# Performance work log

Hardware: AMD Instinct MI355X
Metric: run time of the kernel (lower is better)

The kernel has to match this reference:

```python
import jax, jax.numpy as jnp
import numpy as np

EPS = 1e-5

def layer_norm(x, gamma, beta):
    mu = jnp.mean(x, axis=-1, keepdims=True)
    var = jnp.var(x, axis=-1, keepdims=True)
    return (x - mu) * jax.lax.rsqrt(var + EPS) * gamma + beta

def setup_inputs() -> dict:
    key = jax.random.key(0)
    ks = jax.random.split(key, 9)
    B, S, H = 4, 4096, 1024
    x = jax.random.normal(ks[0], (B, S, H), dtype=jnp.float32)
    w1 = jax.random.normal(ks[1], (H, 4 * H), dtype=jnp.float32) * (1.0 / np.sqrt(H))
    b1 = jnp.zeros((4 * H,), dtype=jnp.float32)
    w2 = jax.random.normal(ks[2], (4 * H, H), dtype=jnp.float32) * (1.0 / np.sqrt(4 * H))
    b2 = jnp.zeros((H,), dtype=jnp.float32)
    g1 = jnp.ones((H,), dtype=jnp.float32)
    be1 = jnp.zeros((H,), dtype=jnp.float32)
    g2 = jnp.ones((H,), dtype=jnp.float32)
    be2 = jnp.zeros((H,), dtype=jnp.float32)
    return {"x": x, "w1": w1, "b1": b1, "w2": w2, "b2": b2,
            "g1": g1, "be1": be1, "g2": g2, "be2": be2}

def reference(x, w1, b1, w2, b2, g1, be1, g2, be2):
    # FNet mixing: FFT over hidden dim, then seq dim, take real part
    x_ft = jnp.fft.fft(jnp.fft.fft(x.astype(jnp.float32), axis=-1), axis=-2).real
    h = layer_norm(x + x_ft, g1, be1)
    # FFN with exact GELU (torch nn.GELU default); dropout is identity in eval
    ffn = jax.nn.gelu(h @ w1 + b1, approximate=False) @ w2 + b2
    return layer_norm(h + ffn, g2, be2)
```

## Files before the change

kernel.cpp:

```cpp
#include <hip/hip_runtime.h>
#include <math.h>
#include <stdint.h>

#define DI __device__ __forceinline__
typedef unsigned short u16;
typedef unsigned int   u32;
typedef unsigned long long u64;

typedef __attribute__((ext_vector_type(4))) float f32x4;
typedef __attribute__((ext_vector_type(8))) short bf16x8;

DI float bf2f(u16 v){ return __uint_as_float(((u32)v) << 16); }
DI u16 f2bf(float f){ u32 u = __float_as_uint(f); return (u16)((u + 0x7FFFu + ((u >> 16) & 1u)) >> 16); }
DI u32 pack2(float re, float im){ return (u32)f2bf(re) | ((u32)f2bf(im) << 16); }

DI float gelu_fast(float v){
  float t = v * v;
  float z = v * fmaf(0.0356774081f, t, 0.7978845608f);
  z = fminf(z, 15.0f);
  float e = __expf(2.0f * z);
  return v * e * __frcp_rn(1.0f + e);
}

__global__ __launch_bounds__(256) void transpose_u32(const u32* __restrict__ in, u32* __restrict__ out, int R, int C){
  __shared__ u32 tile[64][65];
  int t = threadIdx.x;
  int c = t & 63, r0 = t >> 6;
  size_t bofs = (size_t)blockIdx.z * (size_t)R * (size_t)C;
  const u32* ib = in  + bofs + (size_t)(blockIdx.y * 64) * C + blockIdx.x * 64;
  u32*       ob = out + bofs + (size_t)(blockIdx.x * 64) * R + blockIdx.y * 64;
  #pragma unroll
  for (int i = 0; i < 16; i++){ int r = r0 + i * 4; tile[r][c] = ib[(size_t)r * C + c]; }
  __syncthreads();
  #pragma unroll
  for (int i = 0; i < 16; i++){ int r = r0 + i * 4; ob[(size_t)r * R + c] = tile[c][r]; }
}

__global__ __launch_bounds__(256) void transpose_f32_bf16(const float* __restrict__ in, u16* __restrict__ out, int R, int C){
  __shared__ u16 tile[64][65];
  int t = threadIdx.x;
  int c = t & 63, r0 = t >> 6;
  const float* ib = in  + (size_t)(blockIdx.y * 64) * C + blockIdx.x * 64;
  u16*         ob = out + (size_t)(blockIdx.x * 64) * R + blockIdx.y * 64;
  #pragma unroll
  for (int i = 0; i < 16; i++){ int r = r0 + i * 4; tile[r][c] = f2bf(ib[(size_t)r * C + c]); }
  __syncthreads();
  #pragma unroll
  for (int i = 0; i < 16; i++){ int r = r0 + i * 4; ob[(size_t)r * R + c] = tile[c][r]; }
}

template<int LOGN>
DI float2* fft_r4(float2* s, float2* d, int t){
  const int Q = 1 << (LOGN - 2);
  #pragma unroll
  for (int st = 0; st < (LOGN >> 1); ++st){
    const int m = 1 << (2 * st);
    const float ang = -6.28318530717958647692f * (float)m / (float)(1 << LOGN);
    #pragma unroll
    for (int j0 = 0; j0 < Q; j0 += 256){
      int j = j0 + t;
      int p = j >> (2 * st);
      int q = j & (m - 1);
      int o = q + (p << (2 * st + 2));
      float2 a0 = s[j], a1 = s[j + Q], a2 = s[j + 2 * Q], a3 = s[j + 3 * Q];
      float s0r = a0.x + a2.x, s0i = a0.y + a2.y, d0r = a0.x - a2.x, d0i = a0.y - a2.y;
      float s1r = a1.x + a3.x, s1i = a1.y + a3.y, d1r = a1.x - a3.x, d1i = a1.y - a3.y;
      float sn, cs; __sincosf(ang * (float)p, &sn, &cs);
      float t2r = cs * cs - sn * sn, t2i = 2.f * cs * sn;
      float t3r = t2r * cs - t2i * sn, t3i = t2r * sn + t2i * cs;
      float e1r = d0r + d1i, e1i = d0i - d1r;
      float e2r = s0r - s1r, e2i = s0i - s1i;
      float e3r = d0r - d1i, e3i = d0i + d1r;
      d[o]         = make_float2(s0r + s1r, s0i + s1i);
      d[o + m]     = make_float2(cs * e1r - sn * e1i,  cs * e1i + sn * e1r);
      d[o + 2 * m] = make_float2(t2r * e2r - t2i * e2i, t2r * e2i + t2i * e2r);
      d[o + 3 * m] = make_float2(t3r * e3r - t3i * e3i, t3r * e3i + t3i * e3r);
    }
    __syncthreads();
    float2* tp = s; s = d; d = tp;
  }
  return s;
}

__global__ __launch_bounds__(256) void fft_seq(const float* __restrict__ xT, u32* __restrict__ ZT2,
                                               float* __restrict__ Zny){
  __shared__ float2 A[4096], Bb[4096];
  int t = threadIdx.x, g = blockIdx.x;
  const float* r0 = xT + (size_t)(2 * g) * 4096;
  #pragma unroll
  for (int i = 0; i < 4; i++){
    int idx = i * 1024 + t * 4;
    float4 va = *(const float4*)(r0 + idx);
    float4 vb = *(const float4*)(r0 + 4096 + idx);
    A[idx + 0] = make_float2(va.x, vb.x);
    A[idx + 1] = make_float2(va.y, vb.y);
    A[idx + 2] = make_float2(va.z, vb.z);
    A[idx + 3] = make_float2(va.w, vb.w);
  }
  __syncthreads();
  float2* R = fft_r4<12>(A, Bb, t);
  size_t ob0 = (size_t)(2 * g) * 2048;
  #pragma unroll
  for (int i = 0; i < 2; i++){
    int k0 = i * 1024 + t * 4;
    u32 wa[4], wb[4];
    #pragma unroll
    for (int kk = 0; kk < 4; kk++){
      int k = k0 + kk, m = (4096 - k) & 4095;
      float2 zk = R[k], zm = R[m];
      wa[kk] = pack2(0.5f * (zk.x + zm.x), 0.5f * (zk.y - zm.y));
      wb[kk] = pack2(0.5f * (zk.y + zm.y), 0.5f * (zm.x - zk.x));
    }
    *(uint4*)(ZT2 + ob0 + k0)        = make_uint4(wa[0], wa[1], wa[2], wa[3]);
    *(uint4*)(ZT2 + ob0 + 2048 + k0) = make_uint4(wb[0], wb[1], wb[2], wb[3]);
  }
  if (t == 0){ float2 z = R[2048]; Zny[2 * g] = z.x; Zny[2 * g + 1] = z.y; }
}

DI void block_stats4(float a1, float a2, float b1, float b2, int t,
                     float& mA, float& iA, float& mB, float& iB){
  __shared__ float sh[4][4];
  #pragma unroll
  for (int o = 32; o > 0; o >>= 1){
    a1 += __shfl_down(a1, o); a2 += __shfl_down(a2, o);
    b1 += __shfl_down(b1, o); b2 += __shfl_down(b2, o);
  }
  if ((t & 63) == 0){ int w = t >> 6; sh[w][0] = a1; sh[w][1] = a2; sh[w][2] = b1; sh[w][3] = b2; }
  __syncthreads();
  float SA = sh[0][0] + sh[1][0] + sh[2][0] + sh[3][0];
  float QA = sh[0][1] + sh[1][1] + sh[2][1] + sh[3][1];
  float SB = sh[0][2] + sh[1][2] + sh[2][2] + sh[3][2];
  float QB = sh[0][3] + sh[1][3] + sh[2][3] + sh[3][3];
  mA = SA * (1.f / 1024.f); iA = rsqrtf(QA * (1.f / 1024.f) - mA * mA + 1e-5f);
  mB = SB * (1.f / 1024.f); iB = rsqrtf(QB * (1.f / 1024.f) - mB * mB + 1e-5f);
}

__global__ __launch_bounds__(256) void fft_hid_ln(const u32* __restrict__ Z2, const float* __restrict__ Zny,
    const float* __restrict__ x, const float* __restrict__ g1, const float* __restrict__ be1,
    u16* __restrict__ h){
  __shared__ float2 A[1024], Bb[1024];
  int t = threadIdx.x, id = blockIdx.x;
  int b = id / 2049, k = id - b * 2049;
  int idx = t * 4;
  if (k == 2048){
    float4 v = *(const float4*)(Zny + b * 1024 + idx);
    A[idx + 0] = make_float2(v.x, 0.f); A[idx + 1] = make_float2(v.y, 0.f);
    A[idx + 2] = make_float2(v.z, 0.f); A[idx + 3] = make_float2(v.w, 0.f);
  } else {
    uint4 zv = *(const uint4*)(Z2 + ((size_t)b * 2048 + k) * 1024 + idx);
    A[idx + 0] = make_float2(bf2f((u16)(zv.x & 0xffffu)), bf2f((u16)(zv.x >> 16)));
    A[idx + 1] = make_float2(bf2f((u16)(zv.y & 0xffffu)), bf2f((u16)(zv.y >> 16)));
    A[idx + 2] = make_float2(bf2f((u16)(zv.z & 0xffffu)), bf2f((u16)(zv.z >> 16)));
    A[idx + 3] = make_float2(bf2f((u16)(zv.w & 0xffffu)), bf2f((u16)(zv.w >> 16)));
  }
  __syncthreads();
  float2* R = fft_r4<10>(A, Bb, t);
  int rowA = b * 4096 + k;
  bool two = (k >= 1) && (k <= 2047);
  int rowB = b * 4096 + (4096 - k);
  float4 xa = *(const float4*)(x + (size_t)rowA * 1024 + idx);
  float vA0 = R[idx + 0].x + xa.x, vA1 = R[idx + 1].x + xa.y;
  float vA2 = R[idx + 2].x + xa.z, vA3 = R[idx + 3].x + xa.w;
  float vB0 = 0.f, vB1 = 0.f, vB2 = 0.f, vB3 = 0.f;
  if (two){
    float4 xb = *(const float4*)(x + (size_t)rowB * 1024 + idx);
    vB0 = R[(1024 - (idx + 0)) & 1023].x + xb.x;
    vB1 = R[(1024 - (idx + 1)) & 1023].x + xb.y;
    vB2 = R[(1024 - (idx + 2)) & 1023].x + xb.z;
    vB3 = R[(1024 - (idx + 3)) & 1023].x + xb.w;
  }
  float mA, iA, mB, iB;
  block_stats4(vA0 + vA1 + vA2 + vA3, vA0 * vA0 + vA1 * vA1 + vA2 * vA2 + vA3 * vA3,
               vB0 + vB1 + vB2 + vB3, vB0 * vB0 + vB1 * vB1 + vB2 * vB2 + vB3 * vB3,
               t, mA, iA, mB, iB);
  float4 gv = *(const float4*)(g1 + idx);
  float4 bv = *(const float4*)(be1 + idx);
  ushort4 oA;
  oA.x = f2bf((vA0 - mA) * iA * gv.x + bv.x);
  oA.y = f2bf((vA1 - mA) * iA * gv.y + bv.y);
  oA.z = f2bf((vA2 - mA) * iA * gv.z + bv.z);
  oA.w = f2bf((vA3 - mA) * iA * gv.w + bv.w);
  *(ushort4*)(h + (size_t)rowA * 1024 + idx) = oA;
  if (two){
    ushort4 oB;
    oB.x = f2bf((vB0 - mB) * iB * gv.x + bv.x);
    oB.y = f2bf((vB1 - mB) * iB * gv.y + bv.y);
    oB.z = f2bf((vB2 - mB) * iB * gv.z + bv.z);
    oB.w = f2bf((vB3 - mB) * iB * gv.w + bv.w);
    *(ushort4*)(h + (size_t)rowB * 1024 + idx) = oB;
  }
}

__global__ __launch_bounds__(256) void ln_rows(const u16* __restrict__ yv, const float* __restrict__ g,
    const float* __restrict__ be, float* __restrict__ o){
  int t = threadIdx.x;
  size_t base = (size_t)blockIdx.x * 1024;
  int idx = t * 4;
  ushort4 v4 = *(const ushort4*)(yv + base + idx);
  float v0 = bf2f(v4.x), v1 = bf2f(v4.y), v2 = bf2f(v4.z), v3 = bf2f(v4.w);
  float mA, iA, mB, iB;
  block_stats4(v0 + v1 + v2 + v3, v0 * v0 + v1 * v1 + v2 * v2 + v3 * v3, 0.f, 0.f, t, mA, iA, mB, iB);
  float4 gv = *(const float4*)(g + idx);
  float4 bv = *(const float4*)(be + idx);
  float4 ov;
  ov.x = (v0 - mA) * iA * gv.x + bv.x;
  ov.y = (v1 - mA) * iA * gv.y + bv.y;
  ov.z = (v2 - mA) * iA * gv.z + bv.z;
  ov.w = (v3 - mA) * iA * gv.w + bv.w;
  *(float4*)(o + base + idx) = ov;
}

typedef const __attribute__((address_space(1))) void* as1cp;
typedef __attribute__((address_space(3))) void* as3p;
DI void async_copy16(const void* g, void* l){
  __builtin_amdgcn_global_load_lds((as1cp)(u64)g, (as3p)(u32)(u64)l, 16, 0, 0);
}
DI void bar(){
  asm volatile("" ::: "memory");
  __builtin_amdgcn_s_barrier();
  asm volatile("" ::: "memory");
}
DI void stage_unit(const u16* __restrict__ g, int K, int rowbase, int kcol, u16* lds, int wv, int ln){
  #pragma unroll
  for (int i = 0; i < 2; i++){
    int row = wv * 32 + i * 16 + (ln >> 2);
    int gch = (ln & 3) ^ ((row >> 1) & 3);
    async_copy16(g + (size_t)(rowbase + row) * K + kcol + gch * 8,
                 lds + wv * 1024 + i * 512 + ln * 8);
  }
}

template<int DOGELU>
__global__ __launch_bounds__(512, 2) void gemm256(const u16* __restrict__ A, const u16* __restrict__ Bm,
    const float* __restrict__ bias, const u16* __restrict__ resid, u16* __restrict__ C,
    int M, int N, int K, int npg_shift)
{
  __shared__ u16 sA[2][2][8192];
  __shared__ u16 sB[2][2][8192];
  int t = threadIdx.x, wv = t >> 6, ln = t & 63;

  int bid = blockIdx.x;
  int c8 = bid & 7, j = bid >> 3;
  int ng = c8 & 3, mh = c8 >> 2;
  int npg = 1 << npg_shift;
  int mph = (M >> 8) >> 1;
  int n0 = (((ng << npg_shift) + (j & (npg - 1))) << 8);
  int m0 = ((mh * mph + (j >> npg_shift)) << 8);

  int wm = wv >> 2, wn = wv & 3;
  int lt = ln & 15;
  int cs = (((ln >> 4) ^ ((ln >> 1) & 3)) << 3);
  int arow = (wm * 128 + lt) * 32 + cs;
  int brow = (wn * 64 + lt) * 32 + cs;

  f32x4 acc[8][4];
  #pragma unroll
  for (int mf = 0; mf < 8; mf++)
    #pragma unroll
    for (int nf = 0; nf < 4; nf++) acc[mf][nf] = (f32x4){0.f, 0.f, 0.f, 0.f};

  int NT = K >> 6;

  #pragma unroll
  for (int jj = 0; jj < 2; jj++){
    stage_unit(A,  K, m0, jj * 64,      &sA[jj][0][0], wv, ln);
    stage_unit(Bm, K, n0, jj * 64,      &sB[jj][0][0], wv, ln);
    stage_unit(A,  K, m0, jj * 64 + 32, &sA[jj][1][0], wv, ln);
    stage_unit(Bm, K, n0, jj * 64 + 32, &sB[jj][1][0], wv, ln);
  }
  asm volatile("s_waitcnt vmcnt(8)" ::: "memory");
  bar();

  for (int kt = 0; kt < NT; ++kt){
    int buf = kt & 1;
    u16* a0 = &sA[buf][0][0];
    u16* b0 = &sB[buf][0][0];
    bool st = (kt + 2) < NT;
    int kb2 = (kt + 2) << 6;
    bf16x8 af[8], bfr[4];

    #pragma unroll
    for (int mf = 0; mf < 8; mf++) af[mf] = *(const bf16x8*)(a0 + arow + mf * 512);
    #pragma unroll
    for (int nf = 0; nf < 4; nf++) bfr[nf] = *(const bf16x8*)(b0 + brow + nf * 512);
    bar();
    __builtin_amdgcn_s_setprio(1);
    #pragma unroll
    for (int mf = 0; mf < 8; mf++)
      #pragma unroll
      for (int nf = 0; nf < 2; nf++)
        acc[mf][nf] = __builtin_amdgcn_mfma_f32_16x16x32_bf16(af[mf], bfr[nf], acc[mf][nf], 0, 0, 0);
    __builtin_amdgcn_s_setprio(0);
    bar();

    if (st) stage_unit(A, K, m0, kb2, a0, wv, ln);
    bar();
    __builtin_amdgcn_s_setprio(1);
    #pragma unroll
    for (int mf = 0; mf < 8; mf++)
      #pragma unroll
      for (int nf = 2; nf < 4; nf++)
        acc[mf][nf] = __builtin_amdgcn_mfma_f32_16x16x32_bf16(af[mf], bfr[nf], acc[mf][nf], 0, 0, 0);
    __builtin_amdgcn_s_setprio(0);
    bar();

    #pragma unroll
    for (int mf = 0; mf < 8; mf++) af[mf] = *(const bf16x8*)(a0 + 8192 + arow + mf * 512);
    #pragma unroll
    for (int nf = 0; nf < 4; nf++) bfr[nf] = *(const bf16x8*)(b0 + 8192 + brow + nf * 512);
    if (st) stage_unit(Bm, K, n0, kb2, b0, wv, ln);
    bar();
    __builtin_amdgcn_s_setprio(1);
    #pragma unroll
    for (int mf = 0; mf < 8; mf++)
      #pragma unroll
      for (int nf = 0; nf < 2; nf++)
        acc[mf][nf] = __builtin_amdgcn_mfma_f32_16x16x32_bf16(af[mf], bfr[nf], acc[mf][nf], 0, 0, 0);
    __builtin_amdgcn_s_setprio(0);
    asm volatile("s_waitcnt lgkmcnt(0)" ::: "memory");
    bar();

    if (st){
      stage_unit(A,  K, m0, kb2 + 32, a0 + 8192, wv, ln);
      stage_unit(Bm, K, n0, kb2 + 32, b0 + 8192, wv, ln);
    }
    bar();
    __builtin_amdgcn_s_setprio(1);
    #pragma unroll
    for (int mf = 0; mf < 8; mf++)
      #pragma unroll
      for (int nf = 2; nf < 4; nf++)
        acc[mf][nf] = __builtin_amdgcn_mfma_f32_16x16x32_bf16(af[mf], bfr[nf], acc[mf][nf], 0, 0, 0);
    __builtin_amdgcn_s_setprio(0);
    asm volatile("s_waitcnt vmcnt(8)" ::: "memory");
    bar();
  }

  int colq = lt, rq = ln >> 4;
  #pragma unroll
  for (int mf = 0; mf < 8; mf++){
    int mr = m0 + wm * 128 + mf * 16 + rq * 4;
    #pragma unroll
    for (int nf = 0; nf < 4; nf++){
      int col = n0 + wn * 64 + nf * 16 + colq;
      float bv = bias[col];
      #pragma unroll
      for (int i = 0; i < 4; i++){
        float v = acc[mf][nf][i] + bv;
        if (DOGELU){
          v = gelu_fast(v);
        } else {
          v += bf2f(resid[(size_t)(mr + i) * N + col]);
        }
        C[(size_t)(mr + i) * N + col] = f2bf(v);
      }
    }
  }
}

extern "C" void kernel_launch(void* const* d_in, const int* in_sizes, int n_in,
                              void* d_out, int out_size, void* d_ws, size_t ws_size,
                              hipStream_t stream){
  const float* x   = (const float*)d_in[0];
  const float* w1  = (const float*)d_in[1];
  const float* b1  = (const float*)d_in[2];
  const float* w2  = (const float*)d_in[3];
  const float* b2  = (const float*)d_in[4];
  const float* g1  = (const float*)d_in[5];
  const float* be1 = (const float*)d_in[6];
  const float* g2  = (const float*)d_in[7];
  const float* be2 = (const float*)d_in[8];
  float* out = (float*)d_out;
  char* ws = (char*)d_ws;
  const size_t MB = (size_t)1 << 20;
  float* xT  = (float*)(ws);
  u32*  ZT2  = (u32*)(ws + 64 * MB);
  float* Zny = (float*)(ws + 96 * MB);
  u32*  Z2   = (u32*)(ws);
  u16*  h    = (u16*)(ws + 32 * MB);
  u16*  w1T  = (u16*)(ws + 64 * MB);
  u16*  w2T  = (u16*)(ws + 72 * MB);
  u16*  u    = (u16*)(ws + 80 * MB);
  u16*  y    = (u16*)(ws);
  dim3 blk(256, 1, 1);
  dim3 blk2(512, 1, 1);

  transpose_u32<<<dim3(16, 64, 4), blk, 0, stream>>>((const u32*)x, (u32*)xT, 4096, 1024);
  fft_seq      <<<dim3(2048, 1, 1), blk, 0, stream>>>(xT, ZT2, Zny);
  transpose_u32<<<dim3(32, 16, 4), blk, 0, stream>>>(ZT2, Z2, 1024, 2048);
  fft_hid_ln   <<<dim3(4 * 2049, 1, 1), blk, 0, stream>>>(Z2, Zny, x, g1, be1, h);

  transpose_f32_bf16<<<dim3(64, 16, 1), blk, 0, stream>>>(w1, w1T, 1024, 4096);
  transpose_f32_bf16<<<dim3(16, 64, 1), blk, 0, stream>>>(w2, w2T, 4096, 1024);
  int nch = (ws_size >= (size_t)209 * MB) ? 1 : (ws_size >= (size_t)145 * MB) ? 2 : 4;
  int Mc = 16384 / nch;
  for (int ch = 0; ch < nch; ++ch){
    const u16* hch = h + (size_t)ch * Mc * 1024;
    u16* ych = y + (size_t)ch * Mc * 1024;
    gemm256<1><<<dim3((Mc / 256) * 16), blk2, 0, stream>>>(hch, w1T, b1, (const u16*)nullptr, u, Mc, 4096, 1024, 2);
    gemm256<0><<<dim3((Mc / 256) * 4),  blk2, 0, stream>>>(u, w2T, b2, hch, ych, Mc, 1024, 4096, 0);
  }
  ln_rows<<<dim3(16384, 1, 1), blk, 0, stream>>>(y, g2, be2, out);
}
```

Before: 558.9 us.

## Rebalance GEMM async staging across phases and precompute global load addresses

Restructures the GEMM main loop so each of the four phases issues one staging unit. The B half-tile for the next iteration moves earlier, into the first phase, and the B fragments are loaded two at a time just before their MFMAs, which lowers register pressure. Global source pointers and the LDS offset are computed once before the loop instead of per stage call, and the prologue waits on a smaller outstanding count. This spreads memory traffic more evenly over the compute phases and drops one lgkmcnt wait, at the cost of subtler vmcnt bookkeeping and a risk of LDS race bugs.

```diff
diff --git a/kernel.cpp b/kernel.cpp
--- a/kernel.cpp
+++ b/kernel.cpp
@@ -220,15 +220,6 @@
   __builtin_amdgcn_s_barrier();
   asm volatile("" ::: "memory");
 }
-DI void stage_unit(const u16* __restrict__ g, int K, int rowbase, int kcol, u16* lds, int wv, int ln){
-  #pragma unroll
-  for (int i = 0; i < 2; i++){
-    int row = wv * 32 + i * 16 + (ln >> 2);
-    int gch = (ln & 3) ^ ((row >> 1) & 3);
-    async_copy16(g + (size_t)(rowbase + row) * K + kcol + gch * 8,
-                 lds + wv * 1024 + i * 512 + ln * 8);
-  }
-}
 
 template<int DOGELU>
 __global__ __launch_bounds__(512, 2) void gemm256(const u16* __restrict__ A, const u16* __restrict__ Bm,
@@ -253,6 +244,18 @@
   int arow = (wm * 128 + lt) * 32 + cs;
   int brow = (wn * 64 + lt) * 32 + cs;
 
+  int srow = wv * 32 + (ln >> 2);
+  int gch  = ((ln & 3) ^ ((srow >> 1) & 3)) << 3;
+  const u16* gA0 = A  + (size_t)(m0 + srow) * K + gch;
+  const u16* gA1 = gA0 + (size_t)16 * K;
+  const u16* gB0 = Bm + (size_t)(n0 + srow) * K + gch;
+  const u16* gB1 = gB0 + (size_t)16 * K;
+  int ldof = wv * 1024 + ln * 8;
+
+  #define STAGE(g0, g1, kc, unit) do{ \
+    async_copy16((g0) + (kc), (unit) + ldof); \
+    async_copy16((g1) + (kc), (unit) + 512 + ldof); }while(0)
+
   f32x4 acc[8][4];
   #pragma unroll
   for (int mf = 0; mf < 8; mf++)
@@ -261,80 +264,87 @@
 
   int NT = K >> 6;
 
-  #pragma unroll
-  for (int jj = 0; jj < 2; jj++){
-    stage_unit(A,  K, m0, jj * 64,      &sA[jj][0][0], wv, ln);
-    stage_unit(Bm, K, n0, jj * 64,      &sB[jj][0][0], wv, ln);
-    stage_unit(A,  K, m0, jj * 64 + 32, &sA[jj][1][0], wv, ln);
-    stage_unit(Bm, K, n0, jj * 64 + 32, &sB[jj][1][0], wv, ln);
-  }
-  asm volatile("s_waitcnt vmcnt(8)" ::: "memory");
+  STAGE(gA0, gA1, 0,  &sA[0][0][0]);
+  STAGE(gB0, gB1, 0,  &sB[0][0][0]);
+  STAGE(gA0, gA1, 32, &sA[0][1][0]);
+  STAGE(gB0, gB1, 32, &sB[0][1][0]);
+  STAGE(gA0, gA1, 64, &sA[1][0][0]);
+  STAGE(gB0, gB1, 64, &sB[1][0][0]);
+  STAGE(gA0, gA1, 96, &sA[1][1][0]);
+  asm volatile("s_waitcnt vmcnt(6)" ::: "memory");
   bar();
 
   for (int kt = 0; kt < NT; ++kt){
     int buf = kt & 1;
-    u16* a0 = &sA[buf][0][0];
-    u16* b0 = &sB[buf][0][0];
-    bool st = (kt + 2) < NT;
-    int kb2 = (kt + 2) << 6;
-    bf16x8 af[8], bfr[4];
-
-    #pragma unroll
-    for (int mf = 0; mf < 8; mf++) af[mf] = *(const bf16x8*)(a0 + arow + mf * 512);
-    #pragma unroll
-    for (int nf = 0; nf < 4; nf++) bfr[nf] = *(const bf16x8*)(b0 + brow + nf * 512);
+    u16* a0s = &sA[buf][0][0];
+    u16* a1s = &sA[buf][1][0];
+    u16* b0s = &sB[buf][0][0];
+    u16* b1s = &sB[buf][1][0];
+    u16* bn1 = &sB[buf ^ 1][1][0];
+    bool st1 = (kt + 1) < NT;
+    bool st2 = (kt + 2) < NT;
+    int kb1 = (kt + 1) << 6, kb2 = (kt + 2) << 6;
+    bf16x8 af[8], b0r, b1r, b2r, b3r;
+
+    #pragma unroll
+    for (int mf = 0; mf < 8; mf++) af[mf] = *(const bf16x8*)(a0s + arow + mf * 512);
+    b0r = *(const bf16x8*)(b0s + brow);
+    b1r = *(const bf16x8*)(b0s + brow + 512);
+    if (st1) STAGE(gB0, gB1, kb1 + 32, bn1);
     bar();
     __builtin_amdgcn_s_setprio(1);
     #pragma unroll
-    for (int mf = 0; mf < 8; mf++)
-      #pragma unroll
-      for (int nf = 0; nf < 2; nf++)
-        acc[mf][nf] = __builtin_amdgcn_mfma_f32_16x16x32_bf16(af[mf], bfr[nf], acc[mf][nf], 0, 0, 0);
+    for (int mf = 0; mf < 8; mf++){
+      acc[mf][0] = __builtin_amdgcn_mfma_f32_16x16x32_bf16(af[mf], b0r, acc[mf][0], 0, 0, 0);
+      acc[mf][1] = __builtin_amdgcn_mfma_f32_16x16x32_bf16(af[mf], b1r, acc[mf][1], 0, 0, 0);
+    }
     __builtin_amdgcn_s_setprio(0);
     bar();
 
-    if (st) stage_unit(A, K, m0, kb2, a0, wv, ln);
+    b2r = *(const bf16x8*)(b0s + brow + 1024);
+    b3r = *(const bf16x8*)(b0s + brow + 1536);
+    if (st2) STAGE(gA0, gA1, kb2, a0s);
     bar();
     __builtin_amdgcn_s_setprio(1);
     #pragma unroll
-    for (int mf = 0; mf < 8; mf++)
-      #pragma unroll
-      for (int nf = 2; nf < 4; nf++)
-        acc[mf][nf] = __builtin_amdgcn_mfma_f32_16x16x32_bf16(af[mf], bfr[nf], acc[mf][nf], 0, 0, 0);
+    for (int mf = 0; mf < 8; mf++){
+      acc[mf][2] = __builtin_amdgcn_mfma_f32_16x16x32_bf16(af[mf], b2r, acc[mf][2], 0, 0, 0);
+      acc[mf][3] = __builtin_amdgcn_mfma_f32_16x16x32_bf16(af[mf], b3r, acc[mf][3], 0, 0, 0);
+    }
     __builtin_amdgcn_s_setprio(0);
     bar();
 
     #pragma unroll
-    for (int mf = 0; mf < 8; mf++) af[mf] = *(const bf16x8*)(a0 + 8192 + arow + mf * 512);
-    #pragma unroll
-    for (int nf = 0; nf < 4; nf++) bfr[nf] = *(const bf16x8*)(b0 + 8192 + brow + nf * 512);
-    if (st) stage_unit(Bm, K, n0, kb2, b0, wv, ln);
+    for (int mf = 0; mf < 8; mf++) af[mf] = *(const bf16x8*)(a1s + arow + mf * 512);
+    b0r = *(const bf16x8*)(b1s + brow);
+    b1r = *(const bf16x8*)(b1s + brow + 512);
+    if (st2) STAGE(gB0, gB1, kb2, b0s);
     bar();
     __builtin_amdgcn_s_setprio(1);
     #pragma unroll
-    for (int mf = 0; mf < 8; mf++)
-      #pragma unroll
-      for (int nf = 0; nf < 2; nf++)
-        acc[mf][nf] = __builtin_amdgcn_mfma_f32_16x16x32_bf16(af[mf], bfr[nf], acc[mf][nf], 0, 0, 0);
+    for (int mf = 0; mf < 8; mf++){
+      acc[mf][0] = __builtin_amdgcn_mfma_f32_16x16x32_bf16(af[mf], b0r, acc[mf][0], 0, 0, 0);
+      acc[mf][1] = __builtin_amdgcn_mfma_f32_16x16x32_bf16(af[mf], b1r, acc[mf][1], 0, 0, 0);
+    }
     __builtin_amdgcn_s_setprio(0);
-    asm volatile("s_waitcnt lgkmcnt(0)" ::: "memory");
-    bar();
-
-    if (st){
-      stage_unit(A,  K, m0, kb2 + 32, a0 + 8192, wv, ln);
-      stage_unit(Bm, K, n0, kb2 + 32, b0 + 8192, wv, ln);
-    }
+    bar();
+
+    b2r = *(const bf16x8*)(b1s + brow + 1024);
+    b3r = *(const bf16x8*)(b1s + brow + 1536);
+    if (st2) STAGE(gA0, gA1, kb2 + 32, a1s);
     bar();
     __builtin_amdgcn_s_setprio(1);
     #pragma unroll
-    for (int mf = 0; mf < 8; mf++)
-      #pragma unroll
-      for (int nf = 2; nf < 4; nf++)
-        acc[mf][nf] = __builtin_amdgcn_mfma_f32_16x16x32_bf16(af[mf], bfr[nf], acc[mf][nf], 0, 0, 0);
+    for (int mf = 0; mf < 8; mf++){
+      acc[mf][2] = __builtin_amdgcn_mfma_f32_16x16x32_bf16(af[mf], b2r, acc[mf][2], 0, 0, 0);
+      acc[mf][3] = __builtin_amdgcn_mfma_f32_16x16x32_bf16(af[mf], b3r, acc[mf][3], 0, 0, 0);
+    }
     __builtin_amdgcn_s_setprio(0);
-    asm volatile("s_waitcnt vmcnt(8)" ::: "memory");
-    bar();
-  }
+    if (st2) asm volatile("s_waitcnt vmcnt(6)" ::: "memory");
+    else     asm volatile("s_waitcnt vmcnt(0)" ::: "memory");
+    bar();
+  }
+  #undef STAGE
 
   int colq = lt, rq = ln >> 4;
   #pragma unroll
```

Result: no change. 548.5 us (-1.9%).
